# Optimization experiments

Measured on AMD Instinct MI355X. Metric: run time of the kernel, lower is better.

Reference implementation:

```python
import jax, jax.numpy as jnp
import numpy as np

L, B, T, D, H, F, V = 8, 2, 1024, 1024, 16, 4096, 50257


def _ln(x, w, b):
    m = jnp.mean(x, axis=-1, keepdims=True)
    v = jnp.mean((x - m) ** 2, axis=-1, keepdims=True)
    return (x - m) * jax.lax.rsqrt(v + 1e-5) * w + b


def setup_inputs() -> dict:
    key = jax.random.key(0)
    ks = iter(jax.random.split(key, 16))
    s = jnp.float32(0.02)
    w = lambda shape: jax.random.normal(next(ks), shape, jnp.float32) * s
    return {
        'idx': jax.random.randint(next(ks), (B, T), 0, V, jnp.int32),
        'emb': w((V, D)),
        'pos_emb': w((T, D)),
        'ln1_w': jnp.ones((L, D), jnp.float32),
        'ln1_b': jnp.zeros((L, D), jnp.float32),
        'qkv_w': w((L, D, 3 * D)),
        'qkv_b': jnp.zeros((L, 3 * D), jnp.float32),
        'ln2_w': jnp.ones((L, D), jnp.float32),
        'ln2_b': jnp.zeros((L, D), jnp.float32),
        'fc1_w': w((L, D, F)),
        'fc1_b': jnp.zeros((L, F), jnp.float32),
        'fc2_w': w((L, F, D)),
        'fc2_b': jnp.zeros((L, D), jnp.float32),
        'lnf_w': jnp.ones((D,), jnp.float32),
        'lnf_b': jnp.zeros((D,), jnp.float32),
        'head_w': w((D, V)),
        'head_b': jnp.zeros((V,), jnp.float32),
    }


def reference(idx, emb, pos_emb, ln1_w, ln1_b, qkv_w, qkv_b, ln2_w, ln2_b,
              fc1_w, fc1_b, fc2_w, fc2_b, lnf_w, lnf_b, head_w, head_b):
    b, t = idx.shape
    d = emb.shape[1]
    hd = d // H
    x = emb[idx] + pos_emb[:t]                      # [b,t,d]
    mask = jnp.tril(jnp.ones((t, t), bool))         # causal mask
    inv_scale = jnp.float32(1.0 / (d ** 0.5))       # NOTE: source scales by sqrt(full dim), not head_dim

    def layer(x, p):
        l1w, l1b, qw, qb, l2w, l2b, f1w, f1b, f2w, f2b = p
        h = _ln(x, l1w, l1b)
        qkv = h @ qw + qb                           # [b,t,3d]
        q, k, v = jnp.split(qkv, 3, axis=-1)
        q = q.reshape(b, t, H, hd)
        k = k.reshape(b, t, H, hd)
        v = v.reshape(b, t, H, hd)
        logits = jnp.einsum('bqhe,bkhe->bhqk', q, k) * inv_scale
        logits = jnp.where(mask, logits, -jnp.inf)
        attn = jax.nn.softmax(logits, axis=-1)
        o = jnp.einsum('bhqk,bkhe->bqhe', attn, v).reshape(b, t, d)
        x = x + o                                   # no output projection in source
        h = _ln(x, l2w, l2b)
        h = jax.nn.gelu(h @ f1w + f1b, approximate=False)
        h = jax.nn.gelu(h @ f2w + f2b, approximate=False)  # GELU after fc2 too, per source
        return x + h, None

    x, _ = jax.lax.scan(
        layer, x,
        (ln1_w, ln1_b, qkv_w, qkv_b, ln2_w, ln2_b, fc1_w, fc1_b, fc2_w, fc2_b))
    x = _ln(x, lnf_w, lnf_b)
    return x @ head_w + head_b                      # [b,t,V] logits
```

## Files before the change

### kernel.cpp

```cpp
#include <hip/hip_runtime.h>
#include <math.h>

#define Ln 8
#define Bn 2
#define Tn 1024
#define Dm 1024
#define Hn 16
#define Fm 4096
#define Vn 50257
#define NTOK 2048

typedef unsigned short u16;
typedef u16   u16x8  __attribute__((ext_vector_type(8)));
typedef __bf16 bf16x8 __attribute__((ext_vector_type(8)));
typedef float f32x4  __attribute__((ext_vector_type(4)));

__device__ __forceinline__ u16 f2bf(float f){
  unsigned u = __builtin_bit_cast(unsigned, f);
  u += 0x7FFFu + ((u >> 16) & 1u);
  return (u16)(u >> 16);
}
__device__ __forceinline__ float bf2f(u16 s){
  return __builtin_bit_cast(float, ((unsigned)s) << 16);
}
__device__ __forceinline__ float gelu_f(float v){
  return 0.5f * v * (1.0f + erff(v * 0.70710678118654752440f));
}
__device__ __forceinline__ void gload16(const void* g, void* l){
  __builtin_amdgcn_global_load_lds(
      (const __attribute__((address_space(1))) void*)g,
      (__attribute__((address_space(3))) void*)l, 16, 0, 0);
}

__global__ __launch_bounds__(256) void embed_kernel(const int* __restrict__ idx,
                                                    const float* __restrict__ emb,
                                                    const float* __restrict__ pos,
                                                    float* __restrict__ x){
  int row = blockIdx.x;
  int t = row & (Tn - 1);
  int id = idx[row];
  const float4* e = (const float4*)(emb + (size_t)id * Dm);
  const float4* p = (const float4*)(pos + (size_t)t * Dm);
  float4* o = (float4*)(x + (size_t)row * Dm);
  int i = threadIdx.x;
  float4 a = e[i], b = p[i];
  o[i] = make_float4(a.x + b.x, a.y + b.y, a.z + b.z, a.w + b.w);
}

__global__ __launch_bounds__(256) void ln_kernel(const float* __restrict__ xin,
                                                 const float* __restrict__ w,
                                                 const float* __restrict__ bb,
                                                 u16* __restrict__ out){
  int row = blockIdx.x;
  int t = threadIdx.x;
  float4 v = ((const float4*)(xin + (size_t)row * Dm))[t];
  float s  = v.x + v.y + v.z + v.w;
  float s2 = v.x*v.x + v.y*v.y + v.z*v.z + v.w*v.w;
  #pragma unroll
  for (int off = 1; off < 64; off <<= 1){
    s  += __shfl_xor(s, off);
    s2 += __shfl_xor(s2, off);
  }
  __shared__ float red[8];
  int wv = t >> 6, lane = t & 63;
  if (lane == 0){ red[wv] = s; red[4 + wv] = s2; }
  __syncthreads();
  s  = red[0] + red[1] + red[2] + red[3];
  s2 = red[4] + red[5] + red[6] + red[7];
  float mean = s * (1.0f / Dm);
  float var  = s2 * (1.0f / Dm) - mean * mean;
  float rs = rsqrtf(var + 1e-5f);
  float4 wv4 = ((const float4*)w)[t];
  float4 bv4 = ((const float4*)bb)[t];
  u16 o4[4];
  o4[0] = f2bf((v.x - mean) * rs * wv4.x + bv4.x);
  o4[1] = f2bf((v.y - mean) * rs * wv4.y + bv4.y);
  o4[2] = f2bf((v.z - mean) * rs * wv4.z + bv4.z);
  o4[3] = f2bf((v.w - mean) * rs * wv4.w + bv4.w);
  *(uint2*)(out + (size_t)row * Dm + t * 4) = *(uint2*)o4;
}

__device__ __forceinline__ void trans_tile(const float* __restrict__ src,
                                           u16* __restrict__ dst,
                                           int N, int K, int srcCol, int dstRow, int k0){
  __shared__ float tile[64][66];
  int t = threadIdx.x;
  int rr = t >> 4, nc = (t & 15) * 4;
  #pragma unroll
  for (int u = 0; u < 4; u++){
    int kk = rr + u * 16;
    int gn = srcCol + nc;
    const float* sp = src + (size_t)(k0 + kk) * N;
    float4 v;
    if (gn + 3 < N) v = *(const float4*)(sp + gn);
    else {
      v.x = (gn     < N) ? sp[gn]     : 0.0f;
      v.y = (gn + 1 < N) ? sp[gn + 1] : 0.0f;
      v.z = (gn + 2 < N) ? sp[gn + 2] : 0.0f;
      v.w = (gn + 3 < N) ? sp[gn + 3] : 0.0f;
    }
    tile[kk][nc]     = v.x;
    tile[kk][nc + 1] = v.y;
    tile[kk][nc + 2] = v.z;
    tile[kk][nc + 3] = v.w;
  }
  __syncthreads();
  int np = t >> 2, c = t & 3;
  u16* dp = dst + (size_t)(dstRow + np) * K + k0;
  u16 pk[8];
  #pragma unroll
  for (int j = 0; j < 8; j++) pk[j] = f2bf(tile[c*8 + j][np]);
  *(int4*)(dp + c*8) = *(int4*)pk;
  #pragma unroll
  for (int j = 0; j < 8; j++) pk[j] = f2bf(tile[32 + c*8 + j][np]);
  *(int4*)(dp + 32 + c*8) = *(int4*)pk;
}

__global__ __launch_bounds__(256) void transpose_w(const float* __restrict__ Bw,
                                                   u16* __restrict__ Bt,
                                                   int N, int K, int c0){
  int n0 = blockIdx.x * 64, k0 = blockIdx.y * 64;
  trans_tile(Bw, Bt, N, K, c0 + n0, n0, k0);
}

__global__ __launch_bounds__(256) void mega_transpose(const float* __restrict__ qkvw,
                                                      const float* __restrict__ fc1w,
                                                      const float* __restrict__ fc2w,
                                                      const float* __restrict__ headw,
                                                      u16* __restrict__ Wq,
                                                      u16* __restrict__ W1,
                                                      u16* __restrict__ W2,
                                                      u16* __restrict__ Wh){
  int id = blockIdx.x;
  const float* src; u16* dst; int N, K, n0, k0;
  if (id < 6144){
    int l = id / 768, r = id % 768;
    n0 = (r % 48) * 64; k0 = (r / 48) * 64;
    src = qkvw + (size_t)l * Dm * 3072; dst = Wq + (size_t)l * 3072 * Dm;
    N = 3072; K = Dm;
  } else if (id < 14336){
    int id2 = id - 6144;
    int l = id2 / 1024, r = id2 % 1024;
    n0 = (r % 64) * 64; k0 = (r / 64) * 64;
    src = fc1w + (size_t)l * Dm * Fm; dst = W1 + (size_t)l * Fm * Dm;
    N = Fm; K = Dm;
  } else if (id < 22528){
    int id2 = id - 14336;
    int l = id2 / 1024, r = id2 % 1024;
    n0 = (r % 16) * 64; k0 = (r / 16) * 64;
    src = fc2w + (size_t)l * Fm * Dm; dst = W2 + (size_t)l * Dm * Fm;
    N = Dm; K = Fm;
  } else {
    int id2 = id - 22528;
    n0 = (id2 % 786) * 64; k0 = (id2 / 786) * 64;
    src = headw; dst = Wh;
    N = Vn; K = Dm;
  }
  trans_tile(src, dst, N, K, n0, n0, k0);
}

template<int MODE, int BMt, int BNt, int WM, int WN, bool SWZ>
__global__ __launch_bounds__(256) void gemm_kernel(const u16* __restrict__ A,
                                                   const u16* __restrict__ Bt,
                                                   const float* __restrict__ bias,
                                                   void* __restrict__ outp,
                                                   float* __restrict__ resid,
                                                   u16* __restrict__ vT,
                                                   int K, int Nout, int c0){
  constexpr int MR = BMt / (WM * 16);
  constexpr int NR = BNt / (WN * 16);
  __shared__ u16 sA[BMt][64];
  __shared__ u16 sB[BNt][64];
  int t = threadIdx.x;
  int lane = t & 63, w = t >> 6;
  int wm = w / WN, wn = w % WN;
  int lr = lane & 15, lg = lane >> 4;
  int m0, n0;
  if (SWZ){
    int orig = blockIdx.x;
    int q = gridDim.x >> 3;
    int wg = (orig & 7) * q + (orig >> 3);
    m0 = (wg & 15) * BMt;
    n0 = (wg >> 4) * BNt;
  } else {
    m0 = blockIdx.y * BMt; n0 = blockIdx.x * BNt;
  }

  f32x4 acc[MR][NR] = {};

  int srow = lane >> 3, scol = (lane & 7) * 8;
  int cswz = ((lr >> 2) & 3) << 4;

  for (int k0 = 0; k0 < K; k0 += 64){
    __syncthreads();
    #pragma unroll
    for (int i = 0; i < BMt/32; i++){
      int rbase = i*32 + w*8;
      int r = rbase + srow;
      int gc = scol ^ (((r >> 2) & 3) << 4);
      gload16(A + (size_t)(m0 + r) * K + k0 + gc, (char*)&sA[rbase][0]);
    }
    #pragma unroll
    for (int i = 0; i < BNt/32; i++){
      int rbase = i*32 + w*8;
      int r = rbase + srow;
      int gc = scol ^ (((r >> 2) & 3) << 4);
      gload16(Bt + (size_t)(n0 + r) * K + k0 + gc, (char*)&sB[rbase][0]);
    }
    __syncthreads();
    #pragma unroll
    for (int kk = 0; kk < 2; kk++){
      bf16x8 af[MR], bfr[NR];
      #pragma unroll
      for (int i = 0; i < MR; i++) af[i]  = *(const bf16x8*)&sA[wm*(MR*16) + i*16 + lr][(kk*32 + lg*8) ^ cswz];
      #pragma unroll
      for (int j = 0; j < NR; j++) bfr[j] = *(const bf16x8*)&sB[wn*(NR*16) + j*16 + lr][(kk*32 + lg*8) ^ cswz];
      #pragma unroll
      for (int i = 0; i < MR; i++)
        #pragma unroll
        for (int j = 0; j < NR; j++)
          acc[i][j] = __builtin_amdgcn_mfma_f32_16x16x32_bf16(af[i], bfr[j], acc[i][j], 0, 0, 0);
    }
  }

  #pragma unroll
  for (int i = 0; i < MR; i++){
    int gr0 = m0 + wm*(MR*16) + i*16 + lg*4;
    #pragma unroll
    for (int j = 0; j < NR; j++){
      int gc = c0 + n0 + wn*(NR*16) + j*16 + lr;
      if (MODE == 3 && gc >= Nout) continue;
      float bb = bias[gc];
      if (MODE == 0 && gc >= 2048){
        int hh = (gc - 2048) >> 6, dd = (gc - 2048) & 63;
        int b_ = gr0 >> 10, tt = gr0 & 1023;
        u16 pk[4];
        #pragma unroll
        for (int r = 0; r < 4; r++) pk[r] = f2bf(acc[i][j][r] + bb);
        *(uint2*)&vT[((size_t)((b_*Hn + hh)*64 + dd))*Tn + tt] = *(uint2*)pk;
        continue;
      }
      #pragma unroll
      for (int r = 0; r < 4; r++){
        float v = acc[i][j][r] + bb;
        size_t oi = (size_t)(gr0 + r) * Nout + gc;
        if (MODE == 0)      ((u16*)outp)[oi] = f2bf(v);
        else if (MODE == 1) ((u16*)outp)[oi] = f2bf(gelu_f(v));
        else if (MODE == 2) resid[oi] = resid[oi] + gelu_f(v);
        else                ((float*)outp)[oi] = v;
      }
    }
  }
}

__global__ __launch_bounds__(256) void attn_mfma(const u16* __restrict__ qkv,
                                                 const u16* __restrict__ vT,
                                                 float* __restrict__ x){
  int bid = blockIdx.x;
  int bh = bid & 31;
  int j = bid >> 5;
  int qt = (j < 8) ? (15 - j) : (j - 8);
  int b = bh >> 4, h_ = bh & 15;
  int t = threadIdx.x;
  int w = t >> 6, lane = t & 63;
  int lr = lane & 15, lg = lane >> 4;

  __shared__ u16 sK [2][64][72];
  __shared__ u16 sVt[2][64][72];
  __shared__ u16 sP [64][72];

  const u16* qbase = qkv + ((size_t)(b*Tn + qt*64 + w*16 + lr)) * 3*Dm + h_*64 + lg*8;
  bf16x8 qf[2];
  #pragma unroll
  for (int i = 0; i < 2; i++){
    u16x8 raw = *(const u16x8*)(qbase + i * 32);
    #pragma unroll
    for (int u = 0; u < 8; u++) qf[i][u] = (__bf16)(bf2f(raw[u]) * 0.03125f);
  }

  f32x4 o_[4] = {};
  float m_[4], l_[4];
  #pragma unroll
  for (int r = 0; r < 4; r++){ m_[r] = -INFINITY; l_[r] = 0.0f; }

  int sr = t >> 2, scc = (t & 3) * 16;
  const u16* kbase = qkv + ((size_t)(b*Tn + sr)) * 3*Dm + Dm + h_*64 + scc;
  const u16* vbase = vT + ((size_t)(bh*64 + sr)) * Tn + scc;
  int4 kr0, kr1, vr0, vr1;

  kr0 = *(const int4*)(kbase);     kr1 = *(const int4*)(kbase + 8);
  vr0 = *(const int4*)(vbase);     vr1 = *(const int4*)(vbase + 8);
  *(int4*)&sK [0][sr][scc]     = kr0;  *(int4*)&sK [0][sr][scc + 8] = kr1;
  *(int4*)&sVt[0][sr][scc]     = vr0;  *(int4*)&sVt[0][sr][scc + 8] = vr1;

  for (int kt = 0; kt <= qt; kt++){
    int cur = kt & 1;
    if (kt < qt){
      const u16* kb = kbase + (size_t)(kt + 1) * 64 * 3 * Dm;
      const u16* vb = vbase + (kt + 1) * 64;
      kr0 = *(const int4*)(kb);    kr1 = *(const int4*)(kb + 8);
      vr0 = *(const int4*)(vb);    vr1 = *(const int4*)(vb + 8);
    }
    __syncthreads();

    f32x4 s[4] = {};
    __builtin_amdgcn_s_setprio(1);
    #pragma unroll
    for (int kf = 0; kf < 2; kf++){
      #pragma unroll
      for (int nf = 0; nf < 4; nf++){
        bf16x8 kfrag = *(const bf16x8*)&sK[cur][nf*16 + lr][kf*32 + lg*8];
        s[nf] = __builtin_amdgcn_mfma_f32_16x16x32_bf16(qf[kf], kfrag, s[nf], 0, 0, 0);
      }
    }
    __builtin_amdgcn_s_setprio(0);

    bool lastt = (kt == qt);
    float tmax[4] = {-INFINITY, -INFINITY, -INFINITY, -INFINITY};
    #pragma unroll
    for (int nf = 0; nf < 4; nf++)
      #pragma unroll
      for (int r = 0; r < 4; r++){
        float v = s[nf][r];
        if (lastt){
          int kkg = nf*16 + lr, qg = w*16 + lg*4 + r;
          if (kkg > qg) v = -INFINITY;
        }
        s[nf][r] = v;
        tmax[r] = fmaxf(tmax[r], v);
      }
    #pragma unroll
    for (int r = 0; r < 4; r++){
      tmax[r] = fmaxf(tmax[r], __shfl_xor(tmax[r], 1));
      tmax[r] = fmaxf(tmax[r], __shfl_xor(tmax[r], 2));
      tmax[r] = fmaxf(tmax[r], __shfl_xor(tmax[r], 4));
      tmax[r] = fmaxf(tmax[r], __shfl_xor(tmax[r], 8));
    }
    float resc[4], psum[4];
    #pragma unroll
    for (int r = 0; r < 4; r++){
      float nm = fmaxf(m_[r], tmax[r]);
      resc[r] = __expf(m_[r] - nm);
      m_[r] = nm;
      psum[r] = 0.0f;
    }
    #pragma unroll
    for (int nf = 0; nf < 4; nf++)
      #pragma unroll
      for (int r = 0; r < 4; r++){
        float pv = __expf(s[nf][r] - m_[r]);
        s[nf][r] = pv;
        psum[r] += pv;
      }
    #pragma unroll
    for (int r = 0; r < 4; r++){
      psum[r] += __shfl_xor(psum[r], 1);
      psum[r] += __shfl_xor(psum[r], 2);
      psum[r] += __shfl_xor(psum[r], 4);
      psum[r] += __shfl_xor(psum[r], 8);
      l_[r] = l_[r] * resc[r] + psum[r];
    }
    #pragma unroll
    for (int df = 0; df < 4; df++)
      #pragma unroll
      for (int r = 0; r < 4; r++)
        o_[df][r] *= resc[r];

    #pragma unroll
    for (int nf = 0; nf < 4; nf++)
      #pragma unroll
      for (int r = 0; r < 4; r++)
        sP[w*16 + lg*4 + r][nf*16 + lr] = f2bf(s[nf][r]);

    __builtin_amdgcn_s_setprio(1);
    #pragma unroll
    for (int kf = 0; kf < 2; kf++){
      bf16x8 pfrag = *(const bf16x8*)&sP[w*16 + lr][kf*32 + lg*8];
      #pragma unroll
      for (int df = 0; df < 4; df++){
        bf16x8 vfrag = *(const bf16x8*)&sVt[cur][df*16 + lr][kf*32 + lg*8];
        o_[df] = __builtin_amdgcn_mfma_f32_16x16x32_bf16(pfrag, vfrag, o_[df], 0, 0, 0);
      }
    }
    __builtin_amdgcn_s_setprio(0);

    if (kt < qt){
      int nxt = cur ^ 1;
      *(int4*)&sK [nxt][sr][scc]     = kr0;  *(int4*)&sK [nxt][sr][scc + 8] = kr1;
      *(int4*)&sVt[nxt][sr][scc]     = vr0;  *(int4*)&sVt[nxt][sr][scc + 8] = vr1;
    }
  }

  float inv[4];
  #pragma unroll
  for (int r = 0; r < 4; r++) inv[r] = 1.0f / l_[r];
  #pragma unroll
  for (int df = 0; df < 4; df++)
    #pragma unroll
    for (int r = 0; r < 4; r++){
      float* xr = x + ((size_t)(b*Tn + qt*64 + w*16 + lg*4 + r)) * Dm + h_*64 + df*16 + lr;
      *xr += o_[df][r] * inv[r];
    }
}

extern "C" void kernel_launch(void* const* d_in, const int* in_sizes, int n_in,
                              void* d_out, int out_size, void* d_ws, size_t ws_size,
                              hipStream_t stream){
  const int*   idx   = (const int*)  d_in[0];
  const float* emb   = (const float*)d_in[1];
  const float* pos   = (const float*)d_in[2];
  const float* ln1w  = (const float*)d_in[3];
  const float* ln1b  = (const float*)d_in[4];
  const float* qkvw  = (const float*)d_in[5];
  const float* qkvb  = (const float*)d_in[6];
  const float* ln2w  = (const float*)d_in[7];
  const float* ln2b  = (const float*)d_in[8];
  const float* fc1w  = (const float*)d_in[9];
  const float* fc1b  = (const float*)d_in[10];
  const float* fc2w  = (const float*)d_in[11];
  const float* fc2b  = (const float*)d_in[12];
  const float* lnfw  = (const float*)d_in[13];
  const float* lnfb  = (const float*)d_in[14];
  const float* headw = (const float*)d_in[15];
  const float* headb = (const float*)d_in[16];
  float* out = (float*)d_out;

  const size_t MB = 1u << 20;
  char* ws = (char*)d_ws;
  float* x   = (float*)(ws);
  u16*   h   = (u16*)  (ws + 8*MB);
  u16*   qkv = (u16*)  (ws + 12*MB);
  u16*   f1  = (u16*)  (ws + 24*MB);

  bool mega    = ws_size >= 320*MB;
  bool bighead = ws_size >= 116*MB;

  u16 *vT, *Bt = nullptr, *BtF = nullptr, *Wq = nullptr, *W1 = nullptr, *W2 = nullptr, *Wh = nullptr;
  if (mega){
    vT = (u16*)(ws + 40*MB);
    Wq = (u16*)(ws + 44*MB);
    W1 = (u16*)(ws + 92*MB);
    W2 = (u16*)(ws + 156*MB);
    Wh = (u16*)(ws + 220*MB);
  } else {
    Bt  = (u16*)(ws + 40*MB);
    vT  = (u16*)(ws + 48*MB);
    BtF = (u16*)(ws + 12*MB);
  }

  if (mega)
    mega_transpose<<<35104, 256, 0, stream>>>(qkvw, fc1w, fc2w, headw, Wq, W1, W2, Wh);

  embed_kernel<<<NTOK, 256, 0, stream>>>(idx, emb, pos, x);

  for (int l = 0; l < Ln; l++){
    const u16* Bq = mega ? Wq + (size_t)l*3072*Dm : Bt;
    const u16* B1 = mega ? W1 + (size_t)l*Fm*Dm   : Bt;
    const u16* B2 = mega ? W2 + (size_t)l*Dm*Fm   : Bt;
    ln_kernel<<<NTOK, 256, 0, stream>>>(x, ln1w + l*Dm, ln1b + l*Dm, h);
    if (!mega) transpose_w<<<dim3(3072/64, Dm/64), 256, 0, stream>>>(qkvw + (size_t)l*Dm*3072, Bt, 3072, Dm, 0);
    gemm_kernel<0, 64,128,1,4,false><<<dim3(3072/128, NTOK/64), 256, 0, stream>>>(h, Bq, qkvb + l*3072, qkv, nullptr, vT, Dm, 3072, 0);
    attn_mfma<<<512, 256, 0, stream>>>(qkv, vT, x);
    ln_kernel<<<NTOK, 256, 0, stream>>>(x, ln2w + l*Dm, ln2b + l*Dm, h);
    if (!mega) transpose_w<<<dim3(Fm/64, Dm/64), 256, 0, stream>>>(fc1w + (size_t)l*Dm*Fm, Bt, Fm, Dm, 0);
    gemm_kernel<1,128,128,2,2,false><<<dim3(Fm/128, NTOK/128), 256, 0, stream>>>(h, B1, fc1b + l*Fm, f1, nullptr, nullptr, Dm, Fm, 0);
    if (!mega) transpose_w<<<dim3(Dm/64, Fm/64), 256, 0, stream>>>(fc2w + (size_t)l*Fm*Dm, Bt, Dm, Fm, 0);
    gemm_kernel<2, 64,128,1,4,false><<<dim3(Dm/128, NTOK/64), 256, 0, stream>>>(f1, B2, fc2b + l*Dm, nullptr, x, nullptr, Fm, Dm, 0);
  }

  ln_kernel<<<NTOK, 256, 0, stream>>>(x, lnfw, lnfb, h);

  if (mega){
    gemm_kernel<3,128,128,2,2,true><<<6288, 256, 0, stream>>>(h, Wh, headb, out, nullptr, nullptr, Dm, Vn, 0);
  } else if (bighead){
    transpose_w<<<dim3(786, Dm/64), 256, 0, stream>>>(headw, BtF, Vn, Dm, 0);
    gemm_kernel<3,128,128,2,2,true><<<6288, 256, 0, stream>>>(h, BtF, headb, out, nullptr, nullptr, Dm, Vn, 0);
  } else {
    const int CHUNK = 4096;
    for (int c0 = 0; c0 < Vn; c0 += CHUNK){
      int W = Vn - c0; if (W > CHUNK) W = CHUNK;
      int ngx = (W + 127) / 128;
      transpose_w<<<dim3(ngx * 2, Dm/64), 256, 0, stream>>>(headw, Bt, Vn, Dm, c0);
      gemm_kernel<3,128,128,2,2,false><<<dim3(ngx, NTOK/128), 256, 0, stream>>>(h, Bt, headb, out, nullptr, nullptr, Dm, Vn, c0);
    }
  }
}
```

Before: 1.916 ms.

## Add 256x256 double-buffered 8-phase head GEMM and change LDS swizzle

Adds a 512-thread head GEMM that uses 256x256 tiles, double-buffered LDS, and an interleaved 8-phase schedule of loads, LDS reads and MFMAs with explicit barriers and priority hints. The goal is to overlap global loads with compute for the large vocabulary projection. The transposed head weight is padded to 788 column tiles so that the 256-wide N tiles stay in bounds. The generic GEMM's LDS XOR swizzle also changes to a per-row 8-way pattern to reduce bank conflicts. The fine-grained manual waitcnt and barrier choreography carries correctness risk, and the larger tiles leave fewer blocks for the scheduler to balance.

```diff
diff --git a/kernel.cpp b/kernel.cpp
--- a/kernel.cpp
+++ b/kernel.cpp
@@ -152,7 +152,7 @@
     N = Dm; K = Fm;
   } else {
     int id2 = id - 22528;
-    n0 = (id2 % 786) * 64; k0 = (id2 / 786) * 64;
+    n0 = (id2 % 788) * 64; k0 = (id2 / 788) * 64;
     src = headw; dst = Wh;
     N = Vn; K = Dm;
   }
@@ -188,24 +188,21 @@
 
   f32x4 acc[MR][NR] = {};
 
-  int srow = lane >> 3, scol = (lane & 7) * 8;
-  int cswz = ((lr >> 2) & 3) << 4;
+  int srow = lane >> 3;
+  int gcs = ((lane & 7) ^ (lane >> 3)) * 8;
+  int cswz = (lr & 7) << 3;
 
   for (int k0 = 0; k0 < K; k0 += 64){
     __syncthreads();
     #pragma unroll
     for (int i = 0; i < BMt/32; i++){
       int rbase = i*32 + w*8;
-      int r = rbase + srow;
-      int gc = scol ^ (((r >> 2) & 3) << 4);
-      gload16(A + (size_t)(m0 + r) * K + k0 + gc, (char*)&sA[rbase][0]);
+      gload16(A + (size_t)(m0 + rbase + srow) * K + k0 + gcs, (char*)&sA[rbase][0]);
     }
     #pragma unroll
     for (int i = 0; i < BNt/32; i++){
       int rbase = i*32 + w*8;
-      int r = rbase + srow;
-      int gc = scol ^ (((r >> 2) & 3) << 4);
-      gload16(Bt + (size_t)(n0 + r) * K + k0 + gc, (char*)&sB[rbase][0]);
+      gload16(Bt + (size_t)(n0 + rbase + srow) * K + k0 + gcs, (char*)&sB[rbase][0]);
     }
     __syncthreads();
     #pragma unroll
@@ -248,6 +245,116 @@
         else if (MODE == 1) ((u16*)outp)[oi] = f2bf(gelu_f(v));
         else if (MODE == 2) resid[oi] = resid[oi] + gelu_f(v);
         else                ((float*)outp)[oi] = v;
+      }
+    }
+  }
+}
+
+#define BARR() __builtin_amdgcn_s_barrier()
+#define LGK0() asm volatile("s_waitcnt lgkmcnt(0)" ::: "memory")
+#define VMC4() asm volatile("s_waitcnt vmcnt(4)" ::: "memory")
+
+__global__ __launch_bounds__(512) void head_gemm_8ph(const u16* __restrict__ A,
+                                                     const u16* __restrict__ Bw,
+                                                     const float* __restrict__ bias,
+                                                     float* __restrict__ out){
+  __shared__ u16 sA[2][256][64];
+  __shared__ u16 sB[2][256][64];
+  int t = threadIdx.x, lane = t & 63, w = t >> 6;
+  int wm = w >> 2, wn = w & 3;
+  int lr = lane & 15, lg = lane >> 4;
+  int orig = blockIdx.x;
+  int wg = (orig & 7) * (gridDim.x >> 3) + (orig >> 3);
+  int m0g = (wg & 7) << 8;
+  int n0g = (wg >> 3) << 8;
+
+  int srow = w*8 + (lane >> 3);
+  int scol = ((lane & 7) ^ (lane >> 3)) * 8;
+  const u16* Abase = A  + (size_t)(m0g + srow) * 1024 + scol;
+  const u16* Bbase = Bw + (size_t)(n0g + srow) * 1024 + scol;
+
+  f32x4 acc[8][4] = {};
+  bf16x8 a[4][2], b0[2][2], b1[2][2];
+  int rsw = (lr & 7) << 3;
+
+  auto stA = [&](int buf, int half, int tile){
+    const u16* s = Abase + (size_t)half*128*1024 + tile*64;
+    gload16(s,           &sA[buf][half*128 +      w*8][0]);
+    gload16(s + 64*1024, &sA[buf][half*128 + 64 + w*8][0]);
+  };
+  auto stB = [&](int buf, int half, int tile){
+    const u16* s = Bbase + (size_t)half*128*1024 + tile*64;
+    gload16(s,           &sB[buf][half*128 +      w*8][0]);
+    gload16(s + 64*1024, &sB[buf][half*128 + 64 + w*8][0]);
+  };
+  auto rdA = [&](int buf, int half){
+    #pragma unroll
+    for (int i = 0; i < 4; i++)
+      #pragma unroll
+      for (int kk = 0; kk < 2; kk++)
+        a[i][kk] = *(const bf16x8*)&sA[buf][wm*128 + half*64 + i*16 + lr][(kk*32 + lg*8) ^ rsw];
+  };
+  auto rdB = [&](int buf, int half, bf16x8 (&bb)[2][2]){
+    #pragma unroll
+    for (int j = 0; j < 2; j++)
+      #pragma unroll
+      for (int kk = 0; kk < 2; kk++)
+        bb[j][kk] = *(const bf16x8*)&sB[buf][wn*64 + half*32 + j*16 + lr][(kk*32 + lg*8) ^ rsw];
+  };
+  auto MF = [&](int mb, int nb, bf16x8 (&bb)[2][2]){
+    __builtin_amdgcn_s_setprio(1);
+    #pragma unroll
+    for (int kk = 0; kk < 2; kk++)
+      #pragma unroll
+      for (int i = 0; i < 4; i++)
+        #pragma unroll
+        for (int j = 0; j < 2; j++)
+          acc[mb+i][nb+j] = __builtin_amdgcn_mfma_f32_16x16x32_bf16(a[i][kk], bb[j][kk], acc[mb+i][nb+j], 0, 0, 0);
+    __builtin_amdgcn_s_setprio(0);
+  };
+
+  stA(0,0,0); stA(0,1,0); stB(0,0,0); stB(0,1,0);
+  stB(1,0,1); stB(1,1,1);
+  VMC4();
+  BARR();
+
+  for (int it = 0; it < 8; ++it){
+    int T = it * 2;
+    rdA(0,0); rdB(0,0,b0);
+    stA(1,0,T+1);
+    BARR(); LGK0(); MF(0,0,b0); BARR();
+    rdB(0,1,b1);
+    stA(1,1,T+1);
+    BARR(); LGK0(); MF(0,2,b1); BARR();
+    rdA(0,1);
+    if (T+2 < 16) stB(0,0,T+2);
+    BARR(); LGK0(); MF(4,2,b1); BARR();
+    if (T+2 < 16) stB(0,1,T+2);
+    BARR(); MF(4,0,b0); VMC4(); BARR();
+    rdA(1,0); rdB(1,0,b0);
+    if (T+2 < 16) stA(0,0,T+2);
+    BARR(); LGK0(); MF(0,0,b0); BARR();
+    rdB(1,1,b1);
+    if (T+2 < 16) stA(0,1,T+2);
+    BARR(); LGK0(); MF(0,2,b1); BARR();
+    rdA(1,1);
+    if (T+3 < 16) stB(1,0,T+3);
+    BARR(); LGK0(); MF(4,2,b1); BARR();
+    if (T+3 < 16) stB(1,1,T+3);
+    BARR(); MF(4,0,b0); VMC4(); BARR();
+  }
+
+  #pragma unroll
+  for (int m = 0; m < 8; m++){
+    int gr = m0g + wm*128 + m*16 + lg*4;
+    #pragma unroll
+    for (int n = 0; n < 4; n++){
+      int gc = n0g + wn*64 + n*16 + lr;
+      if (gc < Vn){
+        float bb = bias[gc];
+        #pragma unroll
+        for (int r = 0; r < 4; r++)
+          out[(size_t)(gr + r) * Vn + gc] = acc[m][n][r] + bb;
       }
     }
   }
@@ -449,7 +556,7 @@
   }
 
   if (mega)
-    mega_transpose<<<35104, 256, 0, stream>>>(qkvw, fc1w, fc2w, headw, Wq, W1, W2, Wh);
+    mega_transpose<<<35136, 256, 0, stream>>>(qkvw, fc1w, fc2w, headw, Wq, W1, W2, Wh);
 
   embed_kernel<<<NTOK, 256, 0, stream>>>(idx, emb, pos, x);
 
@@ -471,7 +578,7 @@
   ln_kernel<<<NTOK, 256, 0, stream>>>(x, lnfw, lnfb, h);
 
   if (mega){
-    gemm_kernel<3,128,128,2,2,true><<<6288, 256, 0, stream>>>(h, Wh, headb, out, nullptr, nullptr, Dm, Vn, 0);
+    head_gemm_8ph<<<1576, 512, 0, stream>>>(h, Wh, headb, out);
   } else if (bighead){
     transpose_w<<<dim3(786, Dm/64), 256, 0, stream>>>(headw, BtF, Vn, Dm, 0);
     gemm_kernel<3,128,128,2,2,true><<<6288, 256, 0, stream>>>(h, BtF, headb, out, nullptr, nullptr, Dm, Vn, 0);
```

Result: no change. 1.885 ms (-1.6%).
